# Kernel optimization log

Measured on AMD Instinct MI355X. Metric: run time of the kernel, lower is better.

The kernel has to match this reference:

```python
import jax, jax.numpy as jnp
import numpy as np

HEADS = 16
DIM = 1024


def setup_inputs() -> dict:
    key = jax.random.key(0)
    ks = jax.random.split(key, 9)
    b, n, d = 2, 2048, DIM
    scale = 1.0 / np.sqrt(d)  # xavier-ish scale for weights
    x = jax.random.normal(ks[0], (b, n, d), dtype=jnp.float32)
    Wq = jax.random.normal(ks[1], (d, d), dtype=jnp.float32) * scale
    Wk = jax.random.normal(ks[2], (d, d), dtype=jnp.float32) * scale
    Wv = jax.random.normal(ks[3], (d, d), dtype=jnp.float32) * scale
    Wo = jax.random.normal(ks[4], (d, d), dtype=jnp.float32) * scale
    bq = jnp.zeros((d,), jnp.float32)
    bk = jnp.zeros((d,), jnp.float32)
    bv = jnp.zeros((d,), jnp.float32)
    bo = jnp.zeros((d,), jnp.float32)
    return {"x": x, "Wq": Wq, "bq": bq, "Wk": Wk, "bk": bk,
            "Wv": Wv, "bv": bv, "Wo": Wo, "bo": bo}


def reference(x, Wq, bq, Wk, bk, Wv, bv, Wo, bo):
    b, n, d = x.shape
    h = HEADS
    hd = d // h
    # torch Linear: y = x @ W.T + b  (W stored [out, in]; here square so W given as [d,d])
    q = x @ Wq.T + bq
    k = x @ Wk.T + bk
    v = x @ Wv.T + bv
    # b n (h d) -> b h n d
    q = q.reshape(b, n, h, hd).transpose(0, 2, 1, 3)
    k = k.reshape(b, n, h, hd).transpose(0, 2, 1, 3)
    v = v.reshape(b, n, h, hd).transpose(0, 2, 1, 3)
    # NOTE: scale is 1/sqrt(dim), not 1/sqrt(head_dim), faithful to source.
    scores = jnp.einsum('bhqd,bhkd->bhqk', q, k) / jnp.sqrt(jnp.float32(d))
    attn = jax.nn.softmax(scores, axis=-1)
    out = jnp.einsum('bhqk,bhkd->bhqd', attn, v)
    out = out.transpose(0, 2, 1, 3).reshape(b, n, d)  # b h n d -> b n (h d)
    return out @ Wo.T + bo
```

## Files before the change

kernel.cpp:

```cpp
#include <hip/hip_runtime.h>

typedef unsigned short u16t;
typedef __attribute__((ext_vector_type(8))) short bf16x8;
typedef __attribute__((ext_vector_type(4))) float f32x4;

#define DM   1024
#define SEQL 2048
#define NHD  16
#define HDD  64

#define GLL16(g, l) __builtin_amdgcn_global_load_lds( \
    (const __attribute__((address_space(1))) void*)(g), \
    (__attribute__((address_space(3))) void*)(l), 16, 0, 0)

__device__ __forceinline__ u16t f2bf(float f) {
  unsigned u = __float_as_uint(f);
  return (u16t)((u + 0x7fffu + ((u >> 16) & 1u)) >> 16);
}
__device__ __forceinline__ unsigned pack_bf16_2(float a, float b) {
  const unsigned ua = __float_as_uint(a) + 0x8000u;
  const unsigned ub = __float_as_uint(b) + 0x8000u;
  return __builtin_amdgcn_perm(ub, ua, 0x07060302);
}

struct ConvArgs { const float* src[5]; u16t* dst[5]; };

__global__ __launch_bounds__(256) void conv_kernel(ConvArgs a) {
  const int gid = blockIdx.x * 256 + threadIdx.x;
  const int e = gid << 2;
  int sel, off;
  if (e < 4194304) { sel = 0; off = e; }
  else { const int r = e - 4194304; sel = 1 + (r >> 20); off = r & 1048575; }
  const float4 f = *(const float4*)(a.src[sel] + off);
  union { u16t s[4]; uint2 u; } o;
  o.s[0] = f2bf(f.x); o.s[1] = f2bf(f.y); o.s[2] = f2bf(f.z); o.s[3] = f2bf(f.w);
  *(uint2*)(a.dst[sel] + off) = o.u;
}

__device__ __forceinline__ int gslot(int m, int kc) { return (m << 2) + (kc ^ ((m >> 1) & 3)); }

template<int MODE>
__device__ __forceinline__ void qkv_body(
    const u16t* __restrict__ X, const u16t* __restrict__ W,
    const float* __restrict__ bias, float oscale, u16t* __restrict__ outB,
    u16t* smem)
{
  u16t* const Es = smem;

  const int tid = threadIdx.x;
  const int l = tid & 63, w = tid >> 6, q = l >> 4, ln = l & 15;
  const int trow0 = blockIdx.y << 7;
  const int dcol0 = blockIdx.x << 7;
  const int wm = (w >> 1) << 6, wn = (w & 1) << 6;

  const int s0 = (w << 6) + l, s1 = s0 + 256;
  const int m0 = s0 >> 2, kc0 = (s0 & 3) ^ ((m0 >> 1) & 3);
  const int m1 = s1 >> 2, kc1 = (s1 & 3) ^ ((m1 >> 1) & 3);
  const u16t* gA0 = X + (size_t)(trow0 + m0) * DM + (kc0 << 3);
  const u16t* gA1 = X + (size_t)(trow0 + m1) * DM + (kc1 << 3);
  const u16t* gB0 = W + (size_t)(dcol0 + m0) * DM + (kc0 << 3);
  const u16t* gB1 = W + (size_t)(dcol0 + m1) * DM + (kc1 << 3);
  const int dO0 = (w << 6) << 3;
  const int dO1 = ((w << 6) + 256) << 3;

  f32x4 acc[4][4] = {};

  GLL16(gA0, smem + dO0);
  GLL16(gA1, smem + dO1);
  GLL16(gB0, smem + 4096 + dO0);
  GLL16(gB1, smem + 4096 + dO1);

  for (int kt = 0; kt < DM; kt += 32) {
    const int it = kt >> 5;
    u16t* const curA = smem + ((it & 1) ? 8192 : 0);
    u16t* const curB = curA + 4096;
    __syncthreads();
    if (kt + 32 < DM) {
      u16t* const nA = smem + ((it & 1) ? 0 : 8192);
      u16t* const nB = nA + 4096;
      GLL16(gA0 + kt + 32, nA + dO0);
      GLL16(gA1 + kt + 32, nA + dO1);
      GLL16(gB0 + kt + 32, nB + dO0);
      GLL16(gB1 + kt + 32, nB + dO1);
    }

    bf16x8 af[4], bfr[4];
    #pragma unroll
    for (int mi = 0; mi < 4; ++mi) {
      const int r = wm + (mi << 4) + ln;
      af[mi] = *(const bf16x8*)&((MODE == 1 ? curB : curA)[gslot(r, q) << 3]);
    }
    #pragma unroll
    for (int ni = 0; ni < 4; ++ni) {
      const int r = wn + (ni << 4) + ln;
      bfr[ni] = *(const bf16x8*)&((MODE == 1 ? curA : curB)[gslot(r, q) << 3]);
    }
    #pragma unroll
    for (int mi = 0; mi < 4; ++mi)
      #pragma unroll
      for (int ni = 0; ni < 4; ++ni)
        acc[mi][ni] = __builtin_amdgcn_mfma_f32_16x16x32_bf16(af[mi], bfr[ni], acc[mi][ni], 0, 0, 0);
  }

  __syncthreads();

  if (MODE == 1) {
    #pragma unroll
    for (int mi = 0; mi < 4; ++mi) {
      const int dl = wm + (mi << 4) + (q << 2);
      const float4 b4 = *(const float4*)&bias[dcol0 + dl];
      #pragma unroll
      for (int ni = 0; ni < 4; ++ni) {
        const int tl = wn + (ni << 4) + ln;
        uint2 pk;
        pk.x = pack_bf16_2((acc[mi][ni][0] + b4.x) * oscale, (acc[mi][ni][1] + b4.y) * oscale);
        pk.y = pack_bf16_2((acc[mi][ni][2] + b4.z) * oscale, (acc[mi][ni][3] + b4.w) * oscale);
        *(uint2*)&Es[tl * 136 + dl] = pk;
      }
    }
    __syncthreads();
    #pragma unroll
    for (int it = 0; it < 8; ++it) {
      const int u = (it << 8) + tid;
      const int tl = u >> 4, c8 = u & 15;
      const uint4 vv = *(const uint4*)&Es[tl * 136 + (c8 << 3)];
      const int tok = trow0 + tl;
      const int b = tok >> 11, n = tok & (SEQL - 1);
      const int dg = dcol0 + (c8 << 3);
      const int h = dg >> 6, hd = dg & 63;
      *(uint4*)&outB[((size_t)(b * NHD + h) * SEQL + n) * HDD + hd] = vv;
    }
  } else {
    #pragma unroll
    for (int ni = 0; ni < 4; ++ni) {
      const int dl = wn + (ni << 4) + ln;
      const float bv = bias[dcol0 + dl];
      #pragma unroll
      for (int mi = 0; mi < 4; ++mi) {
        const int g = (wm >> 2) + (mi << 2) + q;
        const int g6 = g & 15;
        const int gp = (g & 16) | (g6 & 8) | ((g6 & 3) << 1) | ((g6 >> 2) & 1);
        uint2 pk;
        pk.x = pack_bf16_2(acc[mi][ni][0] + bv, acc[mi][ni][1] + bv);
        pk.y = pack_bf16_2(acc[mi][ni][2] + bv, acc[mi][ni][3] + bv);
        *(uint2*)&Es[dl * 136 + (gp << 2)] = pk;
      }
    }
    __syncthreads();
    #pragma unroll
    for (int it = 0; it < 8; ++it) {
      const int u = (it << 8) + tid;
      const int dl = u >> 4, c8 = u & 15;
      const uint4 vv = *(const uint4*)&Es[dl * 136 + (c8 << 3)];
      const int dg = dcol0 + dl;
      const int h = dg >> 6, hd = dg & 63;
      const int b = trow0 >> 11;
      const int n = (trow0 & (SEQL - 1)) + (c8 << 3);
      *(uint4*)&outB[((size_t)(b * NHD + h) * HDD + hd) * SEQL + n] = vv;
    }
  }
}

struct QKVArgs { const u16t* W[3]; const float* b[3]; u16t* dst[3]; };

__global__ __launch_bounds__(256) void qkv_kernel(const u16t* __restrict__ X, QKVArgs g) {
  __shared__ alignas(16) u16t smem[17408];
  const int z = blockIdx.z;
  if (z == 2)      qkv_body<2>(X, g.W[2], g.b[2], 1.0f, g.dst[2], smem);
  else if (z == 1) qkv_body<1>(X, g.W[1], g.b[1], 1.0f, g.dst[1], smem);
  else             qkv_body<1>(X, g.W[0], g.b[0], 0.03125f, g.dst[0], smem);
}

__global__ __launch_bounds__(256) void outproj_kernel(
    const u16t* __restrict__ A, const u16t* __restrict__ W,
    const float* __restrict__ bias, float* __restrict__ outF)
{
  __shared__ alignas(16) u16t smem[16384];

  const int tid = threadIdx.x;
  const int l = tid & 63, w = tid >> 6, q = l >> 4, ln = l & 15;
  const int row0 = blockIdx.y << 7;
  const int col0 = blockIdx.x << 7;
  const int wm = (w >> 1) << 6, wn = (w & 1) << 6;

  const int s0 = (w << 6) + l, s1 = s0 + 256;
  const int m0 = s0 >> 2, kc0 = (s0 & 3) ^ ((m0 >> 1) & 3);
  const int m1 = s1 >> 2, kc1 = (s1 & 3) ^ ((m1 >> 1) & 3);
  const u16t* gA0 = A + (size_t)(row0 + m0) * DM + (kc0 << 3);
  const u16t* gA1 = A + (size_t)(row0 + m1) * DM + (kc1 << 3);
  const u16t* gB0 = W + (size_t)(col0 + m0) * DM + (kc0 << 3);
  const u16t* gB1 = W + (size_t)(col0 + m1) * DM + (kc1 << 3);
  const int dO0 = (w << 6) << 3;
  const int dO1 = ((w << 6) + 256) << 3;

  f32x4 acc[4][4] = {};

  GLL16(gA0, smem + dO0);
  GLL16(gA1, smem + dO1);
  GLL16(gB0, smem + 4096 + dO0);
  GLL16(gB1, smem + 4096 + dO1);

  for (int kt = 0; kt < DM; kt += 32) {
    const int it = kt >> 5;
    u16t* const curA = smem + ((it & 1) ? 8192 : 0);
    u16t* const curB = curA + 4096;
    __syncthreads();
    if (kt + 32 < DM) {
      u16t* const nA = smem + ((it & 1) ? 0 : 8192);
      u16t* const nB = nA + 4096;
      GLL16(gA0 + kt + 32, nA + dO0);
      GLL16(gA1 + kt + 32, nA + dO1);
      GLL16(gB0 + kt + 32, nB + dO0);
      GLL16(gB1 + kt + 32, nB + dO1);
    }

    bf16x8 af[4], bfr[4];
    #pragma unroll
    for (int mi = 0; mi < 4; ++mi)
      af[mi] = *(const bf16x8*)&curA[gslot(wm + (mi << 4) + ln, q) << 3];
    #pragma unroll
    for (int ni = 0; ni < 4; ++ni)
      bfr[ni] = *(const bf16x8*)&curB[gslot(wn + (ni << 4) + ln, q) << 3];
    #pragma unroll
    for (int mi = 0; mi < 4; ++mi)
      #pragma unroll
      for (int ni = 0; ni < 4; ++ni)
        acc[mi][ni] = __builtin_amdgcn_mfma_f32_16x16x32_bf16(af[mi], bfr[ni], acc[mi][ni], 0, 0, 0);
  }

  #pragma unroll
  for (int ni = 0; ni < 4; ++ni) {
    const int col = col0 + wn + (ni << 4) + ln;
    const float bv = bias[col];
    #pragma unroll
    for (int mi = 0; mi < 4; ++mi)
      #pragma unroll
      for (int r = 0; r < 4; ++r) {
        const int row = row0 + wm + (mi << 4) + (q << 2) + r;
        outF[(size_t)row * DM + col] = acc[mi][ni][r] + bv;
      }
  }
}

__global__ __launch_bounds__(256, 4) void attn_kernel(
    const u16t* __restrict__ Qb, const u16t* __restrict__ Kb,
    const u16t* __restrict__ Vt, u16t* __restrict__ p0,
    u16t* __restrict__ p1, float* __restrict__ ls)
{
  __shared__ alignas(16) u16t smem[16384];

  const int tid = threadIdx.x;
  const int l = tid & 63, w = tid >> 6;
  const int q = l >> 4, ln = l & 15;
  const int bh = blockIdx.y, q0 = blockIdx.x << 7, z = blockIdx.z;
  const int kbase = z << 10;
  const size_t hb = (size_t)bh * SEQL * HDD;
  const u16t* Qg = Qb + hb;
  const u16t* Kg = Kb + hb;
  const u16t* Vg = Vt + hb;

  bf16x8 qf[2][2];
  #pragma unroll
  for (int g = 0; g < 2; ++g) {
    const int qr = q0 + (w << 5) + (g << 4) + ln;
    #pragma unroll
    for (int ks = 0; ks < 2; ++ks)
      qf[g][ks] = *(const bf16x8*)(Qg + (size_t)qr * HDD + (((ks << 2) + q) << 3));
  }

  const int u0 = tid,       r0 = u0 >> 3, c0 = (u0 & 7) ^ (r0 & 7);
  const int u1 = 256 + tid, r1 = u1 >> 3, c1 = (u1 & 7) ^ (r1 & 7);
  const u16t* const kS0 = Kg + (size_t)(kbase + r0) * HDD + (c0 << 3);
  const u16t* const kS1 = Kg + (size_t)(kbase + r1) * HDD + (c1 << 3);
  const u16t* const vS0 = Vg + (size_t)r0 * SEQL + kbase + (c0 << 3);
  const u16t* const vS1 = Vg + (size_t)r1 * SEQL + kbase + (c1 << 3);
  const int dK0 = (w << 6) << 3, dK1 = (256 + (w << 6)) << 3;

  GLL16(kS0, smem + dK0);
  GLL16(kS1, smem + dK1);
  GLL16(vS0, smem + 4096 + dK0);
  GLL16(vS1, smem + 4096 + dK1);

  const short one_s = (short)0x3F80;
  const bf16x8 ones = { one_s, one_s, one_s, one_s, one_s, one_s, one_s, one_s };

  f32x4 accO[2][4] = {};
  f32x4 accL[2] = {};

  for (int t = 0; t < 16; ++t) {
    const int cb = (t & 1) ? 8192 : 0;
    u16t* const Ks = smem + cb;
    u16t* const Vs = smem + cb + 4096;
    __syncthreads();
    if (t + 1 < 16) {
      const int nb = (t & 1) ? 0 : 8192;
      const int ko = (t + 1) << 6;
      GLL16(kS0 + (size_t)ko * HDD, smem + nb + dK0);
      GLL16(kS1 + (size_t)ko * HDD, smem + nb + dK1);
      GLL16(vS0 + ko, smem + nb + 4096 + dK0);
      GLL16(vS1 + ko, smem + nb + 4096 + dK1);
    }

    f32x4 sc[2][4] = {{}, {}};
    #pragma unroll
    for (int ks = 0; ks < 2; ++ks) {
      const int hc = (ks << 2) + q;
      #pragma unroll
      for (int ni = 0; ni < 4; ++ni) {
        const int kr = (ni << 4) + ln;
        const bf16x8 ak = *(const bf16x8*)&Ks[((kr << 3) + (hc ^ (kr & 7))) << 3];
        #pragma unroll
        for (int g = 0; g < 2; ++g)
          sc[g][ni] = __builtin_amdgcn_mfma_f32_16x16x32_bf16(ak, qf[g][ks], sc[g][ni], 0, 0, 0);
      }
    }

    unsigned pk01[2][4], pk23[2][4];
    #pragma unroll
    for (int g = 0; g < 2; ++g)
      #pragma unroll
      for (int ni = 0; ni < 4; ++ni) {
        const float e0 = __expf(sc[g][ni][0]);
        const float e1 = __expf(sc[g][ni][1]);
        const float e2 = __expf(sc[g][ni][2]);
        const float e3 = __expf(sc[g][ni][3]);
        pk01[g][ni] = pack_bf16_2(e0, e1);
        pk23[g][ni] = pack_bf16_2(e2, e3);
      }

    #pragma unroll
    for (int ks = 0; ks < 2; ++ks) {
      union { unsigned u[4]; bf16x8 v; } bfv[2];
      #pragma unroll
      for (int g = 0; g < 2; ++g) {
        bfv[g].u[0] = pk01[g][(ks << 1) + 0];
        bfv[g].u[1] = pk23[g][(ks << 1) + 0];
        bfv[g].u[2] = pk01[g][(ks << 1) + 1];
        bfv[g].u[3] = pk23[g][(ks << 1) + 1];
      }
      #pragma unroll
      for (int g = 0; g < 2; ++g)
        accL[g] = __builtin_amdgcn_mfma_f32_16x16x32_bf16(ones, bfv[g].v, accL[g], 0, 0, 0);
      const int c = (ks << 2) + q;
      #pragma unroll
      for (int nio = 0; nio < 4; ++nio) {
        const int vr = (nio << 4) + ln;
        const bf16x8 av = *(const bf16x8*)&Vs[((vr << 3) + (c ^ (vr & 7))) << 3];
        #pragma unroll
        for (int g = 0; g < 2; ++g)
          accO[g][nio] = __builtin_amdgcn_mfma_f32_16x16x32_bf16(av, bfv[g].v, accO[g][nio], 0, 0, 0);
      }
    }
  }

  if (q == 0) {
    #pragma unroll
    for (int g = 0; g < 2; ++g) {
      const int token = q0 + (w << 5) + (g << 4) + ln;
      ls[(z << 16) + (bh << 11) + token] = accL[g][0];
    }
  }

  __syncthreads();
  #pragma unroll
  for (int g = 0; g < 2; ++g) {
    const int tl = (w << 5) + (g << 4) + ln;
    #pragma unroll
    for (int nio = 0; nio < 4; ++nio) {
      uint2 pk;
      pk.x = pack_bf16_2(accO[g][nio][0], accO[g][nio][1]);
      pk.y = pack_bf16_2(accO[g][nio][2], accO[g][nio][3]);
      *(uint2*)&smem[tl * 72 + (nio << 4) + (q << 2)] = pk;
    }
  }
  __syncthreads();
  u16t* const pbuf = z ? p1 : p0;
  const int h = bh & (NHD - 1), bi = bh >> 4;
  #pragma unroll
  for (int it = 0; it < 4; ++it) {
    const int u = (it << 8) + tid;
    const int tl = u >> 3, c8 = u & 7;
    const uint4 vv = *(const uint4*)&smem[tl * 72 + (c8 << 3)];
    *(uint4*)&pbuf[((size_t)(bi * SEQL + q0 + tl)) * DM + (h << 6) + (c8 << 3)] = vv;
  }
}

__global__ __launch_bounds__(256) void reduce_kernel(
    u16t* __restrict__ p0, const u16t* __restrict__ p1,
    const float* __restrict__ ls)
{
  const int gid = blockIdx.x * 256 + threadIdx.x;
  const int i8 = gid << 3;
  const int ng = i8 >> 10;
  const int d  = i8 & 1023;
  const int h  = d >> 6;
  const int b  = ng >> 11;
  const int n  = ng & (SEQL - 1);
  const int li = (((b << 4) + h) << 11) + n;
  const float inv = 1.0f / (ls[li] + ls[65536 + li]);

  const uint4 a = *(const uint4*)(p0 + i8);
  const uint4 c = *(const uint4*)(p1 + i8);
  uint4 o;
  {
    const unsigned ua[4] = { a.x, a.y, a.z, a.w };
    const unsigned uc[4] = { c.x, c.y, c.z, c.w };
    unsigned uo[4];
    #pragma unroll
    for (int i = 0; i < 4; ++i) {
      const float lo = __uint_as_float(ua[i] << 16) + __uint_as_float(uc[i] << 16);
      const float hi = __uint_as_float(ua[i] & 0xFFFF0000u) + __uint_as_float(uc[i] & 0xFFFF0000u);
      uo[i] = pack_bf16_2(lo * inv, hi * inv);
    }
    o.x = uo[0]; o.y = uo[1]; o.z = uo[2]; o.w = uo[3];
  }
  *(uint4*)(p0 + i8) = o;
}

extern "C" void kernel_launch(void* const* d_in, const int* in_sizes, int n_in,
                              void* d_out, int out_size, void* d_ws, size_t ws_size,
                              hipStream_t stream)
{
  const float* x  = (const float*)d_in[0];
  const float* Wq = (const float*)d_in[1];
  const float* bq = (const float*)d_in[2];
  const float* Wk = (const float*)d_in[3];
  const float* bk = (const float*)d_in[4];
  const float* Wv = (const float*)d_in[5];
  const float* bv = (const float*)d_in[6];
  const float* Wo = (const float*)d_in[7];
  const float* bo = (const float*)d_in[8];
  float* out = (float*)d_out;

  u16t* p = (u16t*)d_ws;
  u16t* xb  = p;  p += 4194304;
  u16t* Wqb = p;  p += 1048576;
  u16t* Wkb = p;  p += 1048576;
  u16t* Wvb = p;  p += 1048576;
  u16t* Wob = p;  p += 1048576;
  u16t* Qbf = p;  p += 4194304;
  u16t* Kbf = p;  p += 4194304;
  u16t* Vtb = p;  p += 4194304;
  u16t* ctx = p;  p += 4194304;

  ConvArgs ca;
  ca.src[0] = x;  ca.dst[0] = xb;
  ca.src[1] = Wq; ca.dst[1] = Wqb;
  ca.src[2] = Wk; ca.dst[2] = Wkb;
  ca.src[3] = Wv; ca.dst[3] = Wvb;
  ca.src[4] = Wo; ca.dst[4] = Wob;
  conv_kernel<<<8192, 256, 0, stream>>>(ca);

  QKVArgs qa;
  qa.W[0] = Wqb; qa.W[1] = Wkb; qa.W[2] = Wvb;
  qa.b[0] = bq;  qa.b[1] = bk;  qa.b[2] = bv;
  qa.dst[0] = Qbf; qa.dst[1] = Kbf; qa.dst[2] = Vtb;
  qkv_kernel<<<dim3(8, 32, 3), 256, 0, stream>>>(xb, qa);

  float* lsum = (float*)Wqb;
  attn_kernel<<<dim3(16, 32, 2), 256, 0, stream>>>(Qbf, Kbf, Vtb, ctx, xb, lsum);

  reduce_kernel<<<2048, 256, 0, stream>>>(ctx, xb, lsum);

  outproj_kernel<<<dim3(8, 32), 256, 0, stream>>>(ctx, Wob, bo, out);
}
```

Measured before the change: 191.7 us.

## Fuse split-K attention reduction into output projection and use exp2 softmax

```diff
diff --git a/kernel.cpp b/kernel.cpp
--- a/kernel.cpp
+++ b/kernel.cpp
@@ -13,6 +13,16 @@
     (const __attribute__((address_space(1))) void*)(g), \
     (__attribute__((address_space(3))) void*)(l), 16, 0, 0)
 
+#if defined(__has_builtin)
+#if __has_builtin(__builtin_amdgcn_exp2f)
+#define EXP2(x) __builtin_amdgcn_exp2f(x)
+#else
+#define EXP2(x) exp2f(x)
+#endif
+#else
+#define EXP2(x) exp2f(x)
+#endif
+
 __device__ __forceinline__ u16t f2bf(float f) {
   unsigned u = __float_as_uint(f);
   return (u16t)((u + 0x7fffu + ((u >> 16) & 1u)) >> 16);
@@ -21,6 +31,11 @@
   const unsigned ua = __float_as_uint(a) + 0x8000u;
   const unsigned ub = __float_as_uint(b) + 0x8000u;
   return __builtin_amdgcn_perm(ub, ua, 0x07060302);
+}
+__device__ __forceinline__ unsigned addpk(unsigned a, unsigned c, float inv) {
+  const float lo = __uint_as_float(a << 16) + __uint_as_float(c << 16);
+  const float hi = __uint_as_float(a & 0xFFFF0000u) + __uint_as_float(c & 0xFFFF0000u);
+  return pack_bf16_2(lo * inv, hi * inv);
 }
 
 struct ConvArgs { const float* src[5]; u16t* dst[5]; };
@@ -168,78 +183,7 @@
   const int z = blockIdx.z;
   if (z == 2)      qkv_body<2>(X, g.W[2], g.b[2], 1.0f, g.dst[2], smem);
   else if (z == 1) qkv_body<1>(X, g.W[1], g.b[1], 1.0f, g.dst[1], smem);
-  else             qkv_body<1>(X, g.W[0], g.b[0], 0.03125f, g.dst[0], smem);
-}
-
-__global__ __launch_bounds__(256) void outproj_kernel(
-    const u16t* __restrict__ A, const u16t* __restrict__ W,
-    const float* __restrict__ bias, float* __restrict__ outF)
-{
-  __shared__ alignas(16) u16t smem[16384];
-
-  const int tid = threadIdx.x;
-  const int l = tid & 63, w = tid >> 6, q = l >> 4, ln = l & 15;
-  const int row0 = blockIdx.y << 7;
-  const int col0 = blockIdx.x << 7;
-  const int wm = (w >> 1) << 6, wn = (w & 1) << 6;
-
-  const int s0 = (w << 6) + l, s1 = s0 + 256;
-  const int m0 = s0 >> 2, kc0 = (s0 & 3) ^ ((m0 >> 1) & 3);
-  const int m1 = s1 >> 2, kc1 = (s1 & 3) ^ ((m1 >> 1) & 3);
-  const u16t* gA0 = A + (size_t)(row0 + m0) * DM + (kc0 << 3);
-  const u16t* gA1 = A + (size_t)(row0 + m1) * DM + (kc1 << 3);
-  const u16t* gB0 = W + (size_t)(col0 + m0) * DM + (kc0 << 3);
-  const u16t* gB1 = W + (size_t)(col0 + m1) * DM + (kc1 << 3);
-  const int dO0 = (w << 6) << 3;
-  const int dO1 = ((w << 6) + 256) << 3;
-
-  f32x4 acc[4][4] = {};
-
-  GLL16(gA0, smem + dO0);
-  GLL16(gA1, smem + dO1);
-  GLL16(gB0, smem + 4096 + dO0);
-  GLL16(gB1, smem + 4096 + dO1);
-
-  for (int kt = 0; kt < DM; kt += 32) {
-    const int it = kt >> 5;
-    u16t* const curA = smem + ((it & 1) ? 8192 : 0);
-    u16t* const curB = curA + 4096;
-    __syncthreads();
-    if (kt + 32 < DM) {
-      u16t* const nA = smem + ((it & 1) ? 0 : 8192);
-      u16t* const nB = nA + 4096;
-      GLL16(gA0 + kt + 32, nA + dO0);
-      GLL16(gA1 + kt + 32, nA + dO1);
-      GLL16(gB0 + kt + 32, nB + dO0);
-      GLL16(gB1 + kt + 32, nB + dO1);
-    }
-
-    bf16x8 af[4], bfr[4];
-    #pragma unroll
-    for (int mi = 0; mi < 4; ++mi)
-      af[mi] = *(const bf16x8*)&curA[gslot(wm + (mi << 4) + ln, q) << 3];
-    #pragma unroll
-    for (int ni = 0; ni < 4; ++ni)
-      bfr[ni] = *(const bf16x8*)&curB[gslot(wn + (ni << 4) + ln, q) << 3];
-    #pragma unroll
-    for (int mi = 0; mi < 4; ++mi)
-      #pragma unroll
-      for (int ni = 0; ni < 4; ++ni)
-        acc[mi][ni] = __builtin_amdgcn_mfma_f32_16x16x32_bf16(af[mi], bfr[ni], acc[mi][ni], 0, 0, 0);
-  }
-
-  #pragma unroll
-  for (int ni = 0; ni < 4; ++ni) {
-    const int col = col0 + wn + (ni << 4) + ln;
-    const float bv = bias[col];
-    #pragma unroll
-    for (int mi = 0; mi < 4; ++mi)
-      #pragma unroll
-      for (int r = 0; r < 4; ++r) {
-        const int row = row0 + wm + (mi << 4) + (q << 2) + r;
-        outF[(size_t)row * DM + col] = acc[mi][ni][r] + bv;
-      }
-  }
+  else             qkv_body<1>(X, g.W[0], g.b[0], 0.04508422f, g.dst[0], smem);
 }
 
 __global__ __launch_bounds__(256, 4) void attn_kernel(
@@ -320,10 +264,10 @@
     for (int g = 0; g < 2; ++g)
       #pragma unroll
       for (int ni = 0; ni < 4; ++ni) {
-        const float e0 = __expf(sc[g][ni][0]);
-        const float e1 = __expf(sc[g][ni][1]);
-        const float e2 = __expf(sc[g][ni][2]);
-        const float e3 = __expf(sc[g][ni][3]);
+        const float e0 = EXP2(sc[g][ni][0]);
+        const float e1 = EXP2(sc[g][ni][1]);
+        const float e2 = EXP2(sc[g][ni][2]);
+        const float e3 = EXP2(sc[g][ni][3]);
         pk01[g][ni] = pack_bf16_2(e0, e1);
         pk23[g][ni] = pack_bf16_2(e2, e3);
       }
@@ -385,36 +329,108 @@
   }
 }
 
-__global__ __launch_bounds__(256) void reduce_kernel(
-    u16t* __restrict__ p0, const u16t* __restrict__ p1,
-    const float* __restrict__ ls)
+__global__ __launch_bounds__(256) void outproj_kernel(
+    const u16t* __restrict__ p0, const u16t* __restrict__ p1,
+    const float* __restrict__ ls, const u16t* __restrict__ W,
+    const float* __restrict__ bias, float* __restrict__ outF)
 {
-  const int gid = blockIdx.x * 256 + threadIdx.x;
-  const int i8 = gid << 3;
-  const int ng = i8 >> 10;
-  const int d  = i8 & 1023;
-  const int h  = d >> 6;
-  const int b  = ng >> 11;
-  const int n  = ng & (SEQL - 1);
-  const int li = (((b << 4) + h) << 11) + n;
-  const float inv = 1.0f / (ls[li] + ls[65536 + li]);
-
-  const uint4 a = *(const uint4*)(p0 + i8);
-  const uint4 c = *(const uint4*)(p1 + i8);
-  uint4 o;
+  __shared__ alignas(16) u16t smem[16384];
+  float* const invS = (float*)(smem + 12288);
+
+  const int tid = threadIdx.x;
+  const int l = tid & 63, w = tid >> 6, q = l >> 4, ln = l & 15;
+  const int row0 = blockIdx.y << 7;
+  const int col0 = blockIdx.x << 6;
+  const int wm = (w >> 1) << 6, wn = (w & 1) << 5;
+
+  #pragma unroll
+  for (int i = 0; i < 8; ++i) {
+    const int idx = (tid << 3) + i;
+    const int tok = row0 + (idx >> 4), h = idx & 15;
+    const int li = ((((tok >> 11) << 4) + h) << 11) + (tok & (SEQL - 1));
+    invS[idx] = 1.0f / (ls[li] + ls[65536 + li]);
+  }
+
+  const int m0 = tid >> 2,         kc0 = (tid & 3) ^ ((m0 >> 1) & 3);
+  const int m1 = (tid + 256) >> 2, kc1 = ((tid + 256) & 3) ^ ((m1 >> 1) & 3);
+  const u16t* const a00 = p0 + (size_t)(row0 + m0) * DM + (kc0 << 3);
+  const u16t* const a01 = p1 + (size_t)(row0 + m0) * DM + (kc0 << 3);
+  const u16t* const a10 = p0 + (size_t)(row0 + m1) * DM + (kc1 << 3);
+  const u16t* const a11 = p1 + (size_t)(row0 + m1) * DM + (kc1 << 3);
+  const int mB = tid >> 2, kcB = (tid & 3) ^ ((mB >> 1) & 3);
+  const u16t* const gB = W + (size_t)(col0 + mB) * DM + (kcB << 3);
+  const int dBo = (w << 6) << 3;
+
+  uint4 r00 = *(const uint4*)a00, r01 = *(const uint4*)a01;
+  uint4 r10 = *(const uint4*)a10, r11 = *(const uint4*)a11;
+  GLL16(gB, smem + 4096 + dBo);
+  __syncthreads();
   {
-    const unsigned ua[4] = { a.x, a.y, a.z, a.w };
-    const unsigned uc[4] = { c.x, c.y, c.z, c.w };
-    unsigned uo[4];
-    #pragma unroll
-    for (int i = 0; i < 4; ++i) {
-      const float lo = __uint_as_float(ua[i] << 16) + __uint_as_float(uc[i] << 16);
-      const float hi = __uint_as_float(ua[i] & 0xFFFF0000u) + __uint_as_float(uc[i] & 0xFFFF0000u);
-      uo[i] = pack_bf16_2(lo * inv, hi * inv);
-    }
-    o.x = uo[0]; o.y = uo[1]; o.z = uo[2]; o.w = uo[3];
-  }
-  *(uint4*)(p0 + i8) = o;
+    const float inv0 = invS[m0 << 4];
+    const float inv1 = invS[m1 << 4];
+    uint4 o0, o1;
+    o0.x = addpk(r00.x, r01.x, inv0); o0.y = addpk(r00.y, r01.y, inv0);
+    o0.z = addpk(r00.z, r01.z, inv0); o0.w = addpk(r00.w, r01.w, inv0);
+    o1.x = addpk(r10.x, r11.x, inv1); o1.y = addpk(r10.y, r11.y, inv1);
+    o1.z = addpk(r10.z, r11.z, inv1); o1.w = addpk(r10.w, r11.w, inv1);
+    *(uint4*)&smem[tid << 3] = o0;
+    *(uint4*)&smem[(tid + 256) << 3] = o1;
+  }
+  r00 = *(const uint4*)(a00 + 32); r01 = *(const uint4*)(a01 + 32);
+  r10 = *(const uint4*)(a10 + 32); r11 = *(const uint4*)(a11 + 32);
+  __syncthreads();
+
+  f32x4 acc[4][2] = {};
+
+  for (int t = 0; t < 32; ++t) {
+    u16t* const cur = smem + ((t & 1) ? 6144 : 0);
+    if (t + 1 < 32) {
+      u16t* const nxt = smem + ((t & 1) ? 0 : 6144);
+      GLL16(gB + ((t + 1) << 5), nxt + 4096 + dBo);
+      const int h1 = (t + 1) >> 1;
+      const float inv0 = invS[(m0 << 4) + h1];
+      const float inv1 = invS[(m1 << 4) + h1];
+      uint4 o0, o1;
+      o0.x = addpk(r00.x, r01.x, inv0); o0.y = addpk(r00.y, r01.y, inv0);
+      o0.z = addpk(r00.z, r01.z, inv0); o0.w = addpk(r00.w, r01.w, inv0);
+      o1.x = addpk(r10.x, r11.x, inv1); o1.y = addpk(r10.y, r11.y, inv1);
+      o1.z = addpk(r10.z, r11.z, inv1); o1.w = addpk(r10.w, r11.w, inv1);
+      *(uint4*)&nxt[tid << 3] = o0;
+      *(uint4*)&nxt[(tid + 256) << 3] = o1;
+      if (t + 2 < 32) {
+        const int kt2 = (t + 2) << 5;
+        r00 = *(const uint4*)(a00 + kt2); r01 = *(const uint4*)(a01 + kt2);
+        r10 = *(const uint4*)(a10 + kt2); r11 = *(const uint4*)(a11 + kt2);
+      }
+    }
+
+    bf16x8 af[4], bfr[2];
+    #pragma unroll
+    for (int mi = 0; mi < 4; ++mi)
+      af[mi] = *(const bf16x8*)&cur[gslot(wm + (mi << 4) + ln, q) << 3];
+    #pragma unroll
+    for (int ni = 0; ni < 2; ++ni)
+      bfr[ni] = *(const bf16x8*)&cur[4096 + (gslot(wn + (ni << 4) + ln, q) << 3)];
+    #pragma unroll
+    for (int mi = 0; mi < 4; ++mi)
+      #pragma unroll
+      for (int ni = 0; ni < 2; ++ni)
+        acc[mi][ni] = __builtin_amdgcn_mfma_f32_16x16x32_bf16(af[mi], bfr[ni], acc[mi][ni], 0, 0, 0);
+    __syncthreads();
+  }
+
+  #pragma unroll
+  for (int ni = 0; ni < 2; ++ni) {
+    const int col = col0 + wn + (ni << 4) + ln;
+    const float bv = bias[col];
+    #pragma unroll
+    for (int mi = 0; mi < 4; ++mi)
+      #pragma unroll
+      for (int r = 0; r < 4; ++r) {
+        const int row = row0 + wm + (mi << 4) + (q << 2) + r;
+        outF[(size_t)row * DM + col] = acc[mi][ni][r] + bv;
+      }
+  }
 }
 
 extern "C" void kernel_launch(void* const* d_in, const int* in_sizes, int n_in,
@@ -460,7 +476,5 @@
   float* lsum = (float*)Wqb;
   attn_kernel<<<dim3(16, 32, 2), 256, 0, stream>>>(Qbf, Kbf, Vtb, ctx, xb, lsum);
 
-  reduce_kernel<<<2048, 256, 0, stream>>>(ctx, xb, lsum);
-
-  outproj_kernel<<<dim3(8, 32), 256, 0, stream>>>(ctx, Wob, bo, out);
-}
+  outproj_kernel<<<dim3(16, 32), 256, 0, stream>>>(ctx, xb, lsum, Wob, bo, out);
+}
```

Measured after the change: 199.4 us. +4.0%, slower.
